# Kernel optimization log

Hardware: AMD Instinct MI355X
Metric: run time of the kernel (lower is better)

Reference implementation:

```python
import jax, jax.numpy as jnp
import numpy as np

H = 512          # size_half
K = 16           # n_segments
B = 8192         # batch
WIDTH = 1.0 / K  # spline bin width


def setup_inputs() -> dict:
    key = jax.random.key(0)
    ks = jax.random.split(key, 4)
    v_in = jax.random.uniform(ks[0], (B, 2 * H), dtype=jnp.float32)  # config in [0,1]
    log_density = jax.random.normal(ks[1], (B, 1), dtype=jnp.float32)
    W1 = jax.random.normal(ks[2], (H, H), dtype=jnp.float32) * (1.0 / np.sqrt(H))
    b1 = jnp.zeros((H,), dtype=jnp.float32)
    W2 = jax.random.normal(ks[3], (H, H * K), dtype=jnp.float32) * (1.0 / np.sqrt(H))
    b2 = jnp.zeros((H * K,), dtype=jnp.float32)
    return {"v_in": v_in, "log_density": log_density, "W1": W1, "b1": b1, "W2": W2, "b2": b2}


def reference(v_in, log_density, W1, b1, W2, b2):
    # even_sites=True: passive = first half, active = second half
    v_passive = v_in[:, :H]           # [B, H]
    v_active = v_in[:, H:]            # [B, H]

    # FullyConnectedNeuralNetwork: hidden layer + final layer, tanh activation on both
    h = jnp.tanh((v_passive - 0.5) @ W1 + b1)          # [B, H]
    net = jnp.tanh(h @ W2 + b2).reshape(-1, H, K)      # [B, H, K]
    p = jax.nn.softmax(net, axis=2)                    # bin probability masses P_k

    # y-coordinates of knots: CDF of the bin masses, with leading zero
    knots_y = jnp.concatenate(
        [jnp.zeros((p.shape[0], H, 1), p.dtype), jnp.cumsum(p, axis=2)], axis=2
    )                                                  # [B, H, K+1]

    # searchsorted on uniform knots linspace(0,1,K+1), then -1, clamped
    knots_x = jnp.linspace(0.0, 1.0, K + 1, dtype=v_in.dtype)
    k = jnp.clip(jnp.searchsorted(knots_x, v_active, side="left") - 1, 0, K - 1)  # [B, H]

    p_k = jnp.take_along_axis(p, k[..., None], axis=2)[..., 0]        # [B, H]
    y_lo = jnp.take_along_axis(knots_y, k[..., None], axis=2)[..., 0]  # [B, H]

    alpha = (v_active - k.astype(v_in.dtype) * WIDTH) / WIDTH          # [B, H]
    v_out_active = y_lo + alpha * p_k

    v_out = jnp.concatenate([v_passive, v_out_active], axis=1)         # [B, 2H]
    log_density_out = log_density - jnp.sum(jnp.log(p_k), axis=1, keepdims=True)  # [B, 1]
    return v_out, log_density_out
```

## Files before the change

kernel.cpp:

```cpp
#include <hip/hip_runtime.h>
#include <hip/hip_bf16.h>

#define HH   512
#define BB   8192
#define WIDTH (1.0f/16.0f)

typedef __attribute__((ext_vector_type(8))) short  short8;
typedef __attribute__((ext_vector_type(4))) float  floatx4;

typedef const __attribute__((address_space(1))) void* gptr_t;
typedef __attribute__((address_space(3))) void*       lptr_t;

__device__ __forceinline__ void gload_lds16(const void* g, void* l) {
    __builtin_amdgcn_global_load_lds((gptr_t)g, (lptr_t)l, 16, 0, 0);
}

__device__ __forceinline__ float tanh_fast(float x) {
    float e = __expf(2.0f * x);
    return 1.0f - 2.0f * __builtin_amdgcn_rcpf(e + 1.0f);
}

__global__ void prep_all(const float* __restrict__ vin, const float* __restrict__ W1,
                         const float* __restrict__ W2, const float* __restrict__ ld,
                         float* __restrict__ vout, float* __restrict__ ldout,
                         __hip_bfloat16* __restrict__ Abf,
                         __hip_bfloat16* __restrict__ W1T,
                         __hip_bfloat16* __restrict__ W2T) {
    __shared__ float tile[32][33];
    int bid = blockIdx.x, tid = threadIdx.x;
    if (bid < 4352) {
        const float* src;  __hip_bfloat16* dst;  int cols, c0, r0;
        if (bid < 4096) { src = W2; dst = W2T; cols = 8192; c0 = (bid & 255) * 32; r0 = (bid >> 8) * 32; }
        else            { int b = bid - 4096; src = W1; dst = W1T; cols = 512; c0 = (b & 15) * 32; r0 = (b >> 4) * 32; }
        int x = tid & 31, y = tid >> 5;
        #pragma unroll
        for (int i = 0; i < 32; i += 8)
            tile[y + i][x] = src[(size_t)(r0 + y + i) * cols + c0 + x];
        __syncthreads();
        #pragma unroll
        for (int i = 0; i < 32; i += 8)
            dst[(size_t)(c0 + y + i) * 512 + r0 + x] = __float2bfloat16(tile[x][y + i]);
    } else {
        int b = bid - 4352;
        int i = b * 256 + tid;
        int r = i >> 6, c = i & 63;
        const float4* src = (const float4*)(vin + (size_t)r * 1024 + c * 8);
        float4 f0 = src[0], f1 = src[1];
        float4* dst = (float4*)(vout + (size_t)r * 1024 + c * 8);
        dst[0] = f0; dst[1] = f1;
        union { __hip_bfloat16 h[8]; uint4 v; } u;
        u.h[0] = __float2bfloat16(f0.x - 0.5f); u.h[1] = __float2bfloat16(f0.y - 0.5f);
        u.h[2] = __float2bfloat16(f0.z - 0.5f); u.h[3] = __float2bfloat16(f0.w - 0.5f);
        u.h[4] = __float2bfloat16(f1.x - 0.5f); u.h[5] = __float2bfloat16(f1.y - 0.5f);
        u.h[6] = __float2bfloat16(f1.z - 0.5f); u.h[7] = __float2bfloat16(f1.w - 0.5f);
        *(uint4*)(Abf + (size_t)r * 512 + c * 8) = u.v;
        if (tid < 4) { int row = b * 4 + tid; ldout[row] = ld[row]; }
    }
}

__global__ __launch_bounds__(256, 4) void gemm1_kernel(
        const __hip_bfloat16* __restrict__ Abf,
        const __hip_bfloat16* __restrict__ W1T,
        const float* __restrict__ b1,
        __hip_bfloat16* __restrict__ hM) {
    __shared__ short ldsA[64 * 32];
    __shared__ short ldsB[128 * 32];
    int tid = threadIdx.x;
    int lane = tid & 63;
    int wv = tid >> 6, wr = wv >> 1, wc = wv & 1;
    int q = lane >> 4, cx = lane & 15;
    int rowBase = blockIdx.y * 64;
    int colBase = blockIdx.x * 128;
    floatx4 acc[2][4] = {};

    for (int k0 = 0; k0 < HH; k0 += 32) {
        {
            int row = tid >> 2, kc = tid & 3;
            unsigned loff = __builtin_amdgcn_readfirstlane((unsigned)((tid & 192) * 16));
            gload_lds16(Abf + (size_t)(rowBase + row) * HH + k0 + kc * 8, (char*)ldsA + loff);
        }
        #pragma unroll
        for (int j = 0; j < 2; ++j) {
            int i = j * 256 + tid;
            int row = i >> 2, kc = i & 3;
            unsigned loff = __builtin_amdgcn_readfirstlane((unsigned)((j * 256 + (tid & 192)) * 16));
            gload_lds16(W1T + (size_t)(colBase + row) * HH + k0 + kc * 8, (char*)ldsB + loff);
        }
        __syncthreads();
        short8 a[2], b[4];
        #pragma unroll
        for (int mt = 0; mt < 2; ++mt)
            a[mt] = *(const short8*)(ldsA + (wr * 32 + mt * 16 + cx) * 32 + q * 8);
        #pragma unroll
        for (int nt = 0; nt < 4; ++nt)
            b[nt] = *(const short8*)(ldsB + (wc * 64 + nt * 16 + cx) * 32 + q * 8);
        #pragma unroll
        for (int mt = 0; mt < 2; ++mt)
            #pragma unroll
            for (int nt = 0; nt < 4; ++nt)
                acc[mt][nt] = __builtin_amdgcn_mfma_f32_16x16x32_bf16(a[mt], b[nt], acc[mt][nt], 0, 0, 0);
        __syncthreads();
    }

    float b1v[4];
    #pragma unroll
    for (int nt = 0; nt < 4; ++nt) b1v[nt] = b1[colBase + wc * 64 + nt * 16 + cx];
    #pragma unroll
    for (int mt = 0; mt < 2; ++mt)
        #pragma unroll
        for (int nt = 0; nt < 4; ++nt) {
            int col = colBase + wc * 64 + nt * 16 + cx;
            #pragma unroll
            for (int r = 0; r < 4; ++r) {
                int row = rowBase + wr * 32 + mt * 16 + q * 4 + r;
                hM[(size_t)row * HH + col] = __float2bfloat16(tanh_fast(acc[mt][nt][r] + b1v[nt]));
            }
        }
}

__global__ __launch_bounds__(512, 2) void gemm2_kernel(
        const __hip_bfloat16* __restrict__ hM,
        const __hip_bfloat16* __restrict__ W2T,
        const float* __restrict__ b2,
        const float* __restrict__ vin,
        float* __restrict__ vout,
        float* __restrict__ ldout) {
    __shared__ __align__(16) char smem[131072];
    int tid = threadIdx.x;
    int lane = tid & 63;
    int wv = tid >> 6;
    int wr = wv >> 2, wc = wv & 3;
    int q = lane >> 4, cx = lane & 15;

    int bid = blockIdx.x;
    int xcd = bid & 7, w = bid >> 3;
    int by = xcd * 4 + (w & 3);
    int bx = w >> 2;
    int rowBase = by * 256;
    int colBase = bx * 256;

    floatx4 acc[8][4] = {};

    int srow = tid >> 3;
    int skw  = ((tid & 7) ^ (srow & 7)) << 3;
    const __hip_bfloat16* gA0 = hM  + (size_t)(rowBase +       srow) * HH + skw;
    const __hip_bfloat16* gA1 = hM  + (size_t)(rowBase +  64 + srow) * HH + skw;
    const __hip_bfloat16* gA2 = hM  + (size_t)(rowBase + 128 + srow) * HH + skw;
    const __hip_bfloat16* gA3 = hM  + (size_t)(rowBase + 192 + srow) * HH + skw;
    const __hip_bfloat16* gB0 = W2T + (size_t)(colBase +       srow) * HH + skw;
    const __hip_bfloat16* gB1 = W2T + (size_t)(colBase +  64 + srow) * HH + skw;
    const __hip_bfloat16* gB2 = W2T + (size_t)(colBase + 128 + srow) * HH + skw;
    const __hip_bfloat16* gB3 = W2T + (size_t)(colBase + 192 + srow) * HH + skw;
    unsigned l0  = (unsigned)__builtin_amdgcn_readfirstlane((tid & 448) * 16);
    unsigned lo0 = l0;
    unsigned lo1 = l0 + 8192;
    unsigned lo2 = l0 + 16384;
    unsigned lo3 = l0 + 24576;

    {
        char* A0 = smem;
        char* B0 = smem + 65536;
        gload_lds16(gA0, A0 + lo0); gload_lds16(gA1, A0 + lo1);
        gload_lds16(gA2, A0 + lo2); gload_lds16(gA3, A0 + lo3);
        gload_lds16(gB0, B0 + lo0); gload_lds16(gB1, B0 + lo1);
        gload_lds16(gB2, B0 + lo2); gload_lds16(gB3, B0 + lo3);
    }

    for (int t = 0; t < 8; ++t) {
        const short* Ac = (const short*)(smem + (t & 1) * 32768);
        const short* Bc = (const short*)(smem + 65536 + (t & 1) * 32768);
        char* An = smem + ((t & 1) ^ 1) * 32768;
        char* Bn = smem + 65536 + ((t & 1) ^ 1) * 32768;
        int kn = (t + 1) * 64;

        asm volatile("s_waitcnt vmcnt(0)" ::: "memory");
        __builtin_amdgcn_sched_barrier(0);
        __builtin_amdgcn_s_barrier();
        __builtin_amdgcn_sched_barrier(0);

        #pragma unroll
        for (int ph = 0; ph < 4; ++ph) {
            const int kk = ph >> 1, mh = ph & 1;
            short8 a[4], b[4];
            #pragma unroll
            for (int i = 0; i < 4; ++i) {
                int rowA = wr * 128 + (mh * 4 + i) * 16 + cx;
                a[i] = *(const short8*)(Ac + rowA * 64 + (((kk * 4 + q) ^ (cx & 7)) << 3));
            }
            #pragma unroll
            for (int nt = 0; nt < 4; ++nt) {
                int rowB = wc * 64 + nt * 16 + cx;
                b[nt] = *(const short8*)(Bc + rowB * 64 + (((kk * 4 + q) ^ (cx & 7)) << 3));
            }
            if (t < 7) {
                if (ph == 0) {
                    gload_lds16(gA0 + kn, An + lo0); gload_lds16(gA1 + kn, An + lo1);
                    gload_lds16(gA2 + kn, An + lo2); gload_lds16(gA3 + kn, An + lo3);
                } else if (ph == 1) {
                    gload_lds16(gB0 + kn, Bn + lo0); gload_lds16(gB1 + kn, Bn + lo1);
                    gload_lds16(gB2 + kn, Bn + lo2); gload_lds16(gB3 + kn, Bn + lo3);
                }
            }
            __builtin_amdgcn_sched_barrier(0);
            __builtin_amdgcn_s_barrier();
            __builtin_amdgcn_sched_barrier(0);
            __builtin_amdgcn_s_setprio(1);
            #pragma unroll
            for (int i = 0; i < 4; ++i)
                #pragma unroll
                for (int nt = 0; nt < 4; ++nt)
                    acc[mh * 4 + i][nt] = __builtin_amdgcn_mfma_f32_16x16x32_bf16(
                        a[i], b[nt], acc[mh * 4 + i][nt], 0, 0, 0);
            __builtin_amdgcn_s_setprio(0);
            __builtin_amdgcn_sched_barrier(0);
            __builtin_amdgcn_s_barrier();
            __builtin_amdgcn_sched_barrier(0);
        }
    }

    float* ldsE = (float*)smem;
    float* myTile = ldsE + wv * (16 * 68);
    int rowL = lane & 15, gL = lane >> 4;
    float b2v[4];
    #pragma unroll
    for (int nt = 0; nt < 4; ++nt) b2v[nt] = b2[colBase + wc * 64 + nt * 16 + cx];

    #pragma unroll
    for (int m = 0; m < 8; ++m) {
        #pragma unroll
        for (int nt = 0; nt < 4; ++nt)
            #pragma unroll
            for (int r = 0; r < 4; ++r)
                myTile[(q * 4 + r) * 68 + nt * 16 + cx] = acc[m][nt][r] + b2v[nt];
        floatx4 x0 = *(const floatx4*)(myTile + rowL * 68 + gL * 16);
        floatx4 x1 = *(const floatx4*)(myTile + rowL * 68 + gL * 16 + 4);
        floatx4 x2 = *(const floatx4*)(myTile + rowL * 68 + gL * 16 + 8);
        floatx4 x3 = *(const floatx4*)(myTile + rowL * 68 + gL * 16 + 12);
        float xs[16] = { x0[0],x0[1],x0[2],x0[3], x1[0],x1[1],x1[2],x1[3],
                         x2[0],x2[1],x2[2],x2[3], x3[0],x3[1],x3[2],x3[3] };

        int row  = rowBase + wr * 128 + m * 16 + rowL;
        int gAbs = bx * 16 + wc * 4 + gL;
        float v = vin[(size_t)row * 1024 + 512 + gAbs];
        int k = (int)ceilf(v * 16.0f) - 1;
        k = min(15, max(0, k));

        float s = 0.0f, csum = 0.0f, ek = 0.0f;
        #pragma unroll
        for (int j = 0; j < 16; ++j) {
            float e2 = __expf(2.0f * xs[j]);
            float tt = 1.0f - 2.0f * __builtin_amdgcn_rcpf(e2 + 1.0f);
            float e  = __expf(tt);
            csum += (j < k)  ? e : 0.0f;
            ek    = (j == k) ? e : ek;
            s += e;
        }
        float rs = __builtin_amdgcn_rcpf(s);
        float pk  = ek * rs;
        float ylo = csum * rs;
        float alpha = (v - (float)k * WIDTH) * 16.0f;
        vout[(size_t)row * 1024 + 512 + gAbs] = ylo + alpha * pk;

        float logp = __logf(pk);
        logp += __shfl_xor(logp, 16, 64);
        logp += __shfl_xor(logp, 32, 64);
        if (lane < 16) atomicAdd(ldout + row, -logp);
    }
}

extern "C" void kernel_launch(void* const* d_in, const int* in_sizes, int n_in,
                              void* d_out, int out_size, void* d_ws, size_t ws_size,
                              hipStream_t stream) {
    const float* vin = (const float*)d_in[0];
    const float* ld  = (const float*)d_in[1];
    const float* W1  = (const float*)d_in[2];
    const float* b1  = (const float*)d_in[3];
    const float* W2  = (const float*)d_in[4];
    const float* b2  = (const float*)d_in[5];
    float* vout  = (float*)d_out;
    float* ldout = vout + (size_t)BB * 1024;

    char* ws = (char*)d_ws;
    __hip_bfloat16* Abf = (__hip_bfloat16*)(ws);
    __hip_bfloat16* W1T = (__hip_bfloat16*)(ws + 8388608);
    __hip_bfloat16* W2T = (__hip_bfloat16*)(ws + 8912896);
    __hip_bfloat16* hM  = (__hip_bfloat16*)(ws + 17301504);

    prep_all<<<6400, 256, 0, stream>>>(vin, W1, W2, ld, vout, ldout, Abf, W1T, W2T);
    gemm1_kernel<<<dim3(4, 128), 256, 0, stream>>>(Abf, W1T, b1, hM);
    gemm2_kernel<<<1024, 512, 0, stream>>>(hM, W2T, b2, vin, vout, ldout);
}
```

Baseline: 212.3 us.

## Vectorize weight transpose, enlarge gemm1 tiles, issue gemm2 prefetch up front

The weight transpose in prep_all now reads float4 rows and writes four bf16 values at a time through a padded LDS tile. gemm1 moves to 128x128 output tiles with a K step of 64 and XOR-swizzled LDS, which halves the grid and raises data reuse per load. gemm2 issues all next-stage loads at the start of each K iteration, waits with vmcnt(8), and uses one barrier per iteration instead of two per phase. The epilogue tile stride is also changed to 76. The bigger gemm1 tile adds register pressure and leaves fewer blocks, and the prefetch change alters how global loads overlap with MFMA work.

After: 209.3 us. Within noise of the previous version (-1.4%).

```diff
diff --git a/kernel.cpp b/kernel.cpp
--- a/kernel.cpp
+++ b/kernel.cpp
@@ -26,20 +26,25 @@
                          __hip_bfloat16* __restrict__ Abf,
                          __hip_bfloat16* __restrict__ W1T,
                          __hip_bfloat16* __restrict__ W2T) {
-    __shared__ float tile[32][33];
+    __shared__ __align__(16) float tile[32 * 36];
     int bid = blockIdx.x, tid = threadIdx.x;
     if (bid < 4352) {
         const float* src;  __hip_bfloat16* dst;  int cols, c0, r0;
         if (bid < 4096) { src = W2; dst = W2T; cols = 8192; c0 = (bid & 255) * 32; r0 = (bid >> 8) * 32; }
         else            { int b = bid - 4096; src = W1; dst = W1T; cols = 512; c0 = (b & 15) * 32; r0 = (b >> 4) * 32; }
-        int x = tid & 31, y = tid >> 5;
-        #pragma unroll
-        for (int i = 0; i < 32; i += 8)
-            tile[y + i][x] = src[(size_t)(r0 + y + i) * cols + c0 + x];
+        int y  = tid >> 3;
+        int x0 = (tid & 7) * 4;
+        float4 v = *(const float4*)(src + (size_t)(r0 + y) * cols + c0 + x0);
+        *(float4*)(tile + y * 36 + x0) = v;
         __syncthreads();
-        #pragma unroll
-        for (int i = 0; i < 32; i += 8)
-            dst[(size_t)(c0 + y + i) * 512 + r0 + x] = __float2bfloat16(tile[x][y + i]);
+        int n  = tid >> 3;
+        int k4 = (tid & 7) * 4;
+        union { __hip_bfloat16 h[4]; uint2 u; } o;
+        o.h[0] = __float2bfloat16(tile[(k4 + 0) * 36 + n]);
+        o.h[1] = __float2bfloat16(tile[(k4 + 1) * 36 + n]);
+        o.h[2] = __float2bfloat16(tile[(k4 + 2) * 36 + n]);
+        o.h[3] = __float2bfloat16(tile[(k4 + 3) * 36 + n]);
+        *(uint2*)(dst + (size_t)(c0 + n) * 512 + r0 + k4) = o.u;
     } else {
         int b = bid - 4352;
         int i = b * 256 + tid;
@@ -63,42 +68,45 @@
         const __hip_bfloat16* __restrict__ W1T,
         const float* __restrict__ b1,
         __hip_bfloat16* __restrict__ hM) {
-    __shared__ short ldsA[64 * 32];
-    __shared__ short ldsB[128 * 32];
+    __shared__ __align__(16) char smem[32768];
+    short* ldsA = (short*)smem;
+    short* ldsB = (short*)(smem + 16384);
     int tid = threadIdx.x;
     int lane = tid & 63;
     int wv = tid >> 6, wr = wv >> 1, wc = wv & 1;
     int q = lane >> 4, cx = lane & 15;
-    int rowBase = blockIdx.y * 64;
+    int srow = tid >> 3;
+    int skw  = ((tid & 7) ^ (srow & 7)) * 8;
+    int rowBase = blockIdx.y * 128;
     int colBase = blockIdx.x * 128;
-    floatx4 acc[2][4] = {};
-
-    for (int k0 = 0; k0 < HH; k0 += 32) {
-        {
-            int row = tid >> 2, kc = tid & 3;
-            unsigned loff = __builtin_amdgcn_readfirstlane((unsigned)((tid & 192) * 16));
-            gload_lds16(Abf + (size_t)(rowBase + row) * HH + k0 + kc * 8, (char*)ldsA + loff);
-        }
-        #pragma unroll
-        for (int j = 0; j < 2; ++j) {
-            int i = j * 256 + tid;
-            int row = i >> 2, kc = i & 3;
+    floatx4 acc[4][4] = {};
+
+    for (int k0 = 0; k0 < HH; k0 += 64) {
+        #pragma unroll
+        for (int j = 0; j < 4; ++j) {
+            int row = j * 32 + srow;
             unsigned loff = __builtin_amdgcn_readfirstlane((unsigned)((j * 256 + (tid & 192)) * 16));
-            gload_lds16(W1T + (size_t)(colBase + row) * HH + k0 + kc * 8, (char*)ldsB + loff);
+            gload_lds16(Abf + (size_t)(rowBase + row) * HH + k0 + skw, (char*)ldsA + loff);
+            gload_lds16(W1T + (size_t)(colBase + row) * HH + k0 + skw, (char*)ldsB + loff);
         }
         __syncthreads();
-        short8 a[2], b[4];
-        #pragma unroll
-        for (int mt = 0; mt < 2; ++mt)
-            a[mt] = *(const short8*)(ldsA + (wr * 32 + mt * 16 + cx) * 32 + q * 8);
-        #pragma unroll
-        for (int nt = 0; nt < 4; ++nt)
-            b[nt] = *(const short8*)(ldsB + (wc * 64 + nt * 16 + cx) * 32 + q * 8);
-        #pragma unroll
-        for (int mt = 0; mt < 2; ++mt)
+        #pragma unroll
+        for (int s = 0; s < 2; ++s) {
+            short8 a[4], b[4];
+            #pragma unroll
+            for (int mt = 0; mt < 4; ++mt)
+                a[mt] = *(const short8*)(ldsA + (wr * 64 + mt * 16 + cx) * 64
+                                              + (((s * 4 + q) ^ (cx & 7)) << 3));
             #pragma unroll
             for (int nt = 0; nt < 4; ++nt)
-                acc[mt][nt] = __builtin_amdgcn_mfma_f32_16x16x32_bf16(a[mt], b[nt], acc[mt][nt], 0, 0, 0);
+                b[nt] = *(const short8*)(ldsB + (wc * 64 + nt * 16 + cx) * 64
+                                              + (((s * 4 + q) ^ (cx & 7)) << 3));
+            #pragma unroll
+            for (int mt = 0; mt < 4; ++mt)
+                #pragma unroll
+                for (int nt = 0; nt < 4; ++nt)
+                    acc[mt][nt] = __builtin_amdgcn_mfma_f32_16x16x32_bf16(a[mt], b[nt], acc[mt][nt], 0, 0, 0);
+        }
         __syncthreads();
     }
 
@@ -106,13 +114,13 @@
     #pragma unroll
     for (int nt = 0; nt < 4; ++nt) b1v[nt] = b1[colBase + wc * 64 + nt * 16 + cx];
     #pragma unroll
-    for (int mt = 0; mt < 2; ++mt)
+    for (int mt = 0; mt < 4; ++mt)
         #pragma unroll
         for (int nt = 0; nt < 4; ++nt) {
             int col = colBase + wc * 64 + nt * 16 + cx;
             #pragma unroll
             for (int r = 0; r < 4; ++r) {
-                int row = rowBase + wr * 32 + mt * 16 + q * 4 + r;
+                int row = rowBase + wr * 64 + mt * 16 + q * 4 + r;
                 hM[(size_t)row * HH + col] = __float2bfloat16(tanh_fast(acc[mt][nt][r] + b1v[nt]));
             }
         }
@@ -152,28 +160,34 @@
     const __hip_bfloat16* gB2 = W2T + (size_t)(colBase + 128 + srow) * HH + skw;
     const __hip_bfloat16* gB3 = W2T + (size_t)(colBase + 192 + srow) * HH + skw;
     unsigned l0  = (unsigned)__builtin_amdgcn_readfirstlane((tid & 448) * 16);
-    unsigned lo0 = l0;
-    unsigned lo1 = l0 + 8192;
-    unsigned lo2 = l0 + 16384;
-    unsigned lo3 = l0 + 24576;
+    unsigned lo0 = l0, lo1 = l0 + 8192, lo2 = l0 + 16384, lo3 = l0 + 24576;
 
     {
-        char* A0 = smem;
-        char* B0 = smem + 65536;
+        char* A0 = smem;  char* B0 = smem + 65536;
         gload_lds16(gA0, A0 + lo0); gload_lds16(gA1, A0 + lo1);
         gload_lds16(gA2, A0 + lo2); gload_lds16(gA3, A0 + lo3);
         gload_lds16(gB0, B0 + lo0); gload_lds16(gB1, B0 + lo1);
         gload_lds16(gB2, B0 + lo2); gload_lds16(gB3, B0 + lo3);
     }
 
+    #pragma unroll
     for (int t = 0; t < 8; ++t) {
         const short* Ac = (const short*)(smem + (t & 1) * 32768);
         const short* Bc = (const short*)(smem + 65536 + (t & 1) * 32768);
-        char* An = smem + ((t & 1) ^ 1) * 32768;
-        char* Bn = smem + 65536 + ((t & 1) ^ 1) * 32768;
-        int kn = (t + 1) * 64;
-
-        asm volatile("s_waitcnt vmcnt(0)" ::: "memory");
+        if (t < 7) {
+            char* An = smem + ((t + 1) & 1) * 32768;
+            char* Bn = smem + 65536 + ((t + 1) & 1) * 32768;
+            int kn = (t + 1) * 64;
+            gload_lds16(gA0 + kn, An + lo0); gload_lds16(gA1 + kn, An + lo1);
+            gload_lds16(gA2 + kn, An + lo2); gload_lds16(gA3 + kn, An + lo3);
+            gload_lds16(gB0 + kn, Bn + lo0); gload_lds16(gB1 + kn, Bn + lo1);
+            gload_lds16(gB2 + kn, Bn + lo2); gload_lds16(gB3 + kn, Bn + lo3);
+            __builtin_amdgcn_sched_barrier(0);
+            asm volatile("s_waitcnt vmcnt(8)" ::: "memory");
+        } else {
+            __builtin_amdgcn_sched_barrier(0);
+            asm volatile("s_waitcnt vmcnt(0)" ::: "memory");
+        }
         __builtin_amdgcn_sched_barrier(0);
         __builtin_amdgcn_s_barrier();
         __builtin_amdgcn_sched_barrier(0);
@@ -192,18 +206,6 @@
                 int rowB = wc * 64 + nt * 16 + cx;
                 b[nt] = *(const short8*)(Bc + rowB * 64 + (((kk * 4 + q) ^ (cx & 7)) << 3));
             }
-            if (t < 7) {
-                if (ph == 0) {
-                    gload_lds16(gA0 + kn, An + lo0); gload_lds16(gA1 + kn, An + lo1);
-                    gload_lds16(gA2 + kn, An + lo2); gload_lds16(gA3 + kn, An + lo3);
-                } else if (ph == 1) {
-                    gload_lds16(gB0 + kn, Bn + lo0); gload_lds16(gB1 + kn, Bn + lo1);
-                    gload_lds16(gB2 + kn, Bn + lo2); gload_lds16(gB3 + kn, Bn + lo3);
-                }
-            }
-            __builtin_amdgcn_sched_barrier(0);
-            __builtin_amdgcn_s_barrier();
-            __builtin_amdgcn_sched_barrier(0);
             __builtin_amdgcn_s_setprio(1);
             #pragma unroll
             for (int i = 0; i < 4; ++i)
@@ -212,14 +214,14 @@
                     acc[mh * 4 + i][nt] = __builtin_amdgcn_mfma_f32_16x16x32_bf16(
                         a[i], b[nt], acc[mh * 4 + i][nt], 0, 0, 0);
             __builtin_amdgcn_s_setprio(0);
-            __builtin_amdgcn_sched_barrier(0);
-            __builtin_amdgcn_s_barrier();
-            __builtin_amdgcn_sched_barrier(0);
-        }
+        }
+        __builtin_amdgcn_sched_barrier(0);
+        __builtin_amdgcn_s_barrier();
+        __builtin_amdgcn_sched_barrier(0);
     }
 
     float* ldsE = (float*)smem;
-    float* myTile = ldsE + wv * (16 * 68);
+    float* myTile = ldsE + wv * (16 * 76);
     int rowL = lane & 15, gL = lane >> 4;
     float b2v[4];
     #pragma unroll
@@ -231,11 +233,12 @@
         for (int nt = 0; nt < 4; ++nt)
             #pragma unroll
             for (int r = 0; r < 4; ++r)
-                myTile[(q * 4 + r) * 68 + nt * 16 + cx] = acc[m][nt][r] + b2v[nt];
-        floatx4 x0 = *(const floatx4*)(myTile + rowL * 68 + gL * 16);
-        floatx4 x1 = *(const floatx4*)(myTile + rowL * 68 + gL * 16 + 4);
-        floatx4 x2 = *(const floatx4*)(myTile + rowL * 68 + gL * 16 + 8);
-        floatx4 x3 = *(const floatx4*)(myTile + rowL * 68 + gL * 16 + 12);
+                myTile[(q * 4 + r) * 76 + nt * 16 + cx] = acc[m][nt][r] + b2v[nt];
+
+        floatx4 x0 = *(const floatx4*)(myTile + rowL * 76 + gL * 16);
+        floatx4 x1 = *(const floatx4*)(myTile + rowL * 76 + gL * 16 + 4);
+        floatx4 x2 = *(const floatx4*)(myTile + rowL * 76 + gL * 16 + 8);
+        floatx4 x3 = *(const floatx4*)(myTile + rowL * 76 + gL * 16 + 12);
         float xs[16] = { x0[0],x0[1],x0[2],x0[3], x1[0],x1[1],x1[2],x1[3],
                          x2[0],x2[1],x2[2],x2[3], x3[0],x3[1],x3[2],x3[3] };
 
@@ -287,6 +290,6 @@
     __hip_bfloat16* hM  = (__hip_bfloat16*)(ws + 17301504);
 
     prep_all<<<6400, 256, 0, stream>>>(vin, W1, W2, ld, vout, ldout, Abf, W1T, W2T);
-    gemm1_kernel<<<dim3(4, 128), 256, 0, stream>>>(Abf, W1T, b1, hM);
+    gemm1_kernel<<<dim3(4, 64), 256, 0, stream>>>(Abf, W1T, b1, hM);
     gemm2_kernel<<<1024, 512, 0, stream>>>(hM, W2T, b2, vin, vout, ldout);
 }
```
